# Kernel optimization log

Hardware: AMD Instinct MI355X
Metric: run time of the kernel (lower is better)

Reference implementation:

```python
import jax, jax.numpy as jnp
import numpy as np
import math

B, S, D, H, HD, R, F = 2, 2048, 1024, 16, 64, 32, 4096
EPS = 1e-5

def _layernorm(x, g, b):
    mu = jnp.mean(x, axis=-1, keepdims=True)
    var = jnp.mean(jnp.square(x - mu), axis=-1, keepdims=True)
    return (x - mu) * jax.lax.rsqrt(var + EPS) * g + b

def _gelu(x):
    # faithful tanh-approximation from the module
    c = math.sqrt(2.0 / math.pi)
    return 0.5 * x * (1.0 + jnp.tanh(c * (x + 0.044715 * x ** 3)))

def setup_inputs() -> dict:
    key = jax.random.key(0)
    ks = jax.random.split(key, 8)
    s = 0.02
    return dict(
        x=jax.random.normal(ks[0], (B, S, D), jnp.float32),
        ln1_g=jnp.ones((D,), jnp.float32), ln1_b=jnp.zeros((D,), jnp.float32),
        Wq=jax.random.normal(ks[1], (H, D, HD), jnp.float32) * s,
        bq=jnp.zeros((H, HD), jnp.float32),
        Wk=jax.random.normal(ks[2], (H, D, HD), jnp.float32) * s,
        bk=jnp.zeros((H, HD), jnp.float32),
        Wvd=jax.random.normal(ks[3], (H, D, R), jnp.float32) * s,
        bvd=jnp.zeros((H, R), jnp.float32),
        Wvu=jax.random.normal(ks[4], (H, R, HD), jnp.float32) * s,
        bvu=jnp.zeros((H, HD), jnp.float32),
        ln2_g=jnp.ones((D,), jnp.float32), ln2_b=jnp.zeros((D,), jnp.float32),
        W1=jax.random.normal(ks[5], (D, F), jnp.float32) * s,
        b1=jnp.zeros((F,), jnp.float32),
        W2=jax.random.normal(ks[6], (F, D), jnp.float32) * s,
        b2=jnp.zeros((D,), jnp.float32),
    )

def reference(x, ln1_g, ln1_b, Wq, bq, Wk, bk, Wvd, bvd, Wvu, bvu,
              ln2_g, ln2_b, W1, b1, W2, b2):
    Bx, Sx, Dx = x.shape
    y = x
    h = _layernorm(x, ln1_g, ln1_b)
    # all heads batched: [B,H,S,HD]
    q = jnp.einsum('bsd,hde->bhse', h, Wq) + bq[None, :, None, :]
    k = jnp.einsum('bsd,hde->bhse', h, Wk) + bk[None, :, None, :]
    vd = jnp.einsum('bsd,hdr->bhsr', h, Wvd) + bvd[None, :, None, :]
    v = jnp.einsum('bhsr,hre->bhse', vd, Wvu) + bvu[None, :, None, :]
    scores = jnp.einsum('bhse,bhte->bhst', q, k) / math.sqrt(Dx)  # NB: scaled by embed dim, as in source
    i = jnp.arange(Sx)
    mask = i[None, :] < i[:, None]  # key index < query index is masked (reversed causal, faithful)
    scores = jnp.where(mask[None, None, :, :], -jnp.inf, scores)
    attn = jax.nn.softmax(scores, axis=-1)
    o = jnp.einsum('bhst,bhte->bhse', attn, v)
    o = o.transpose(0, 2, 1, 3).reshape(Bx, Sx, Dx)  # concat heads
    x = o + y
    y = x
    h = _layernorm(x, ln2_g, ln2_b)
    h = _gelu(h @ W1 + b1)
    h = h @ W2 + b2
    return h + y
```

## Files before the change

kernel.cpp:

```cpp
#include <hip/hip_runtime.h>


typedef unsigned short u16;
typedef __attribute__((ext_vector_type(4))) float f32x4;
typedef __attribute__((ext_vector_type(8))) __bf16 bf16x8;

#define B_ 2
#define S_ 2048
#define D_ 1024
#define H_ 16
#define HD_ 64
#define R_ 32
#define F_ 4096
#define M_ (B_ * S_)
#define NQKV 2560
#define C2F 0.04508422002778011f

__device__ __forceinline__ u16 f2bf(float f) {
  union { float f; unsigned u; } v; v.f = f;
  unsigned u = v.u;
  return (u16)((u + 0x7FFFu + ((u >> 16) & 1u)) >> 16);
}
__device__ __forceinline__ float bf2f(u16 h) {
  union { unsigned u; float f; } v; v.u = ((unsigned)h) << 16;
  return v.f;
}
__device__ __forceinline__ unsigned pk_bf16(float lo, float hi) {
  unsigned r;
  asm volatile("v_cvt_pk_bf16_f32 %0, %1, %2" : "=v"(r) : "v"(lo), "v"(hi));
  return r;
}

typedef __attribute__((address_space(1))) void gvoid;
typedef __attribute__((address_space(3))) void lvoid;
__device__ __forceinline__ void gload_lds16(const void* g, void* l) {
  __builtin_amdgcn_global_load_lds((gvoid*)(void*)g, (lvoid*)l, 16, 0, 0);
}

__device__ __forceinline__ float gelu_f(float x) {
  float t = tanhf(0.7978845608028654f * (x + 0.044715f * x * x * x));
  return 0.5f * x * (1.0f + t);
}

__global__ __launch_bounds__(256) void wtrans(const float* __restrict__ in,
                                              u16* __restrict__ out,
                                              int Rr, int Cc, long ibs, long obs,
                                              float scale) {
  __shared__ float tile[32][33];
  const float* ip = in + (size_t)blockIdx.z * ibs;
  u16* op = out + (size_t)blockIdx.z * obs;
  int c0 = blockIdx.x * 32, r0 = blockIdx.y * 32;
  int tx = threadIdx.x & 31, ty = threadIdx.x >> 5;
#pragma unroll
  for (int j = 0; j < 32; j += 8)
    tile[ty + j][tx] = ip[(size_t)(r0 + ty + j) * Cc + c0 + tx];
  __syncthreads();
#pragma unroll
  for (int j = 0; j < 32; j += 8)
    op[(size_t)(c0 + ty + j) * Rr + r0 + tx] = f2bf(tile[tx][ty + j] * scale);
}

__global__ __launch_bounds__(256) void wconv(const float* __restrict__ in,
                                             u16* __restrict__ out, int n) {
  int i = (blockIdx.x * 256 + threadIdx.x) * 4;
  if (i < n) {
    float4 v = *(const float4*)&in[i];
    ushort4 o;
    o.x = f2bf(v.x); o.y = f2bf(v.y); o.z = f2bf(v.z); o.w = f2bf(v.w);
    *(ushort4*)&out[i] = o;
  }
}

__global__ __launch_bounds__(256) void bconcat(const float* __restrict__ bq,
                                               const float* __restrict__ bk,
                                               const float* __restrict__ bvd,
                                               float* __restrict__ o) {
  int i = blockIdx.x * 256 + threadIdx.x;
  if (i < NQKV) {
    float v = (i < 1024) ? bq[i] * C2F : (i < 2048 ? bk[i - 1024] : bvd[i - 2048]);
    o[i] = v;
  }
}

__global__ __launch_bounds__(256) void ln_kernel(const float* __restrict__ xin,
                                                 const float* __restrict__ addin,
                                                 const float* __restrict__ gam,
                                                 const float* __restrict__ bet,
                                                 u16* __restrict__ hout,
                                                 float* __restrict__ x2out) {
  int row = blockIdx.x, tid = threadIdx.x;
  size_t base = (size_t)row * D_ + tid * 4;
  float4 v = *(const float4*)&xin[base];
  if (addin) {
    float4 a = *(const float4*)&addin[base];
    v.x += a.x; v.y += a.y; v.z += a.z; v.w += a.w;
  }
  if (x2out) *(float4*)&x2out[base] = v;
  float s = v.x + v.y + v.z + v.w;
  float ss = v.x * v.x + v.y * v.y + v.z * v.z + v.w * v.w;
#pragma unroll
  for (int off = 32; off > 0; off >>= 1) {
    s += __shfl_down(s, off);
    ss += __shfl_down(ss, off);
  }
  __shared__ float red[8];
  int wv = tid >> 6;
  if ((tid & 63) == 0) { red[wv] = s; red[4 + wv] = ss; }
  __syncthreads();
  if (tid == 0) {
    float s1 = red[0] + red[1] + red[2] + red[3];
    float s2 = red[4] + red[5] + red[6] + red[7];
    float mu = s1 * (1.0f / D_);
    red[0] = mu;
    red[1] = s2 * (1.0f / D_) - mu * mu;
  }
  __syncthreads();
  float mu = red[0];
  float rstd = rsqrtf(red[1] + 1e-5f);
  int ci = tid * 4;
  ushort4 o;
  o.x = f2bf((v.x - mu) * rstd * gam[ci + 0] + bet[ci + 0]);
  o.y = f2bf((v.y - mu) * rstd * gam[ci + 1] + bet[ci + 1]);
  o.z = f2bf((v.z - mu) * rstd * gam[ci + 2] + bet[ci + 2]);
  o.w = f2bf((v.w - mu) * rstd * gam[ci + 3] + bet[ci + 3]);
  *(ushort4*)&hout[base] = o;
}

template <int MODE>
__global__ __launch_bounds__(256) void gemm_nt(const u16* __restrict__ A,
                                               const u16* __restrict__ Bt,
                                               int K, int lda, int ldb,
                                               const float* __restrict__ bias,
                                               const float* __restrict__ res,
                                               void* __restrict__ Cout,
                                               void* __restrict__ Cout2, int ldc) {
  __shared__ __align__(16) u16 As0[128 * 32];
  __shared__ __align__(16) u16 Bs0[128 * 32];
  __shared__ __align__(16) u16 As1[128 * 32];
  __shared__ __align__(16) u16 Bs1[128 * 32];
  int tid = threadIdx.x;
  int lane = tid & 63, wid = tid >> 6;
  int wm = wid >> 1, wn = wid & 1;
  int row0 = blockIdx.y * 128, col0 = blockIdx.x * 128;
  int l15 = lane & 15, g = lane >> 4;
  int srow = lane >> 2, scol = (lane & 3) * 8;
  f32x4 acc[4][4] = {};
  const u16* Ap = A + (size_t)row0 * lda;
  const u16* Bp = Bt + (size_t)col0 * ldb;

  auto STAGE = [&](u16* AS, u16* BS, int kk) {
#pragma unroll
    for (int i = 0; i < 2; ++i) {
      int c = wid * 2 + i;
      gload_lds16(Ap + (size_t)(c * 16 + srow) * lda + kk + scol, &AS[c * 512]);
      gload_lds16(Bp + (size_t)(c * 16 + srow) * ldb + kk + scol, &BS[c * 512]);
    }
  };
  auto COMPUTE = [&](const u16* AS, const u16* BS) {
    bf16x8 af[4], bfr[4];
#pragma unroll
    for (int t = 0; t < 4; ++t) {
      af[t] = *(const bf16x8*)&AS[(wm * 64 + t * 16 + l15) * 32 + g * 8];
      bfr[t] = *(const bf16x8*)&BS[(wn * 64 + t * 16 + l15) * 32 + g * 8];
    }
#pragma unroll
    for (int mt = 0; mt < 4; ++mt)
#pragma unroll
      for (int nt = 0; nt < 4; ++nt)
        acc[mt][nt] = __builtin_amdgcn_mfma_f32_16x16x32_bf16(af[mt], bfr[nt],
                                                              acc[mt][nt], 0, 0, 0);
  };

  STAGE(As0, Bs0, 0);
  __syncthreads();
  for (int k0 = 0; k0 < K; k0 += 64) {
    if (k0 + 32 < K) STAGE(As1, Bs1, k0 + 32);
    COMPUTE(As0, Bs0);
    __syncthreads();
    if (k0 + 64 < K) STAGE(As0, Bs0, k0 + 64);
    COMPUTE(As1, Bs1);
    __syncthreads();
  }

#pragma unroll
  for (int mt = 0; mt < 4; ++mt) {
#pragma unroll
    for (int nt = 0; nt < 4; ++nt) {
      int cc = col0 + wn * 64 + nt * 16 + l15;
      float bv = bias ? bias[cc] : 0.0f;
#pragma unroll
      for (int j = 0; j < 4; ++j) {
        int rr = row0 + wm * 64 + mt * 16 + g * 4 + j;
        float v = acc[mt][nt][j] + bv;
        if (MODE == 1) v = gelu_f(v);
        if (MODE == 2) {
          ((float*)Cout)[(size_t)rr * ldc + cc] = v + res[(size_t)rr * ldc + cc];
        } else {
          ((u16*)Cout)[(size_t)rr * ldc + cc] = f2bf(v);
        }
      }
    }
  }
  (void)Cout2;
}

template <int MODE>
__global__ __launch_bounds__(512, 2) void gemm8(
    const u16* __restrict__ A, const u16* __restrict__ Bt,
    int lda, int ldb, int nk,
    const float* __restrict__ bias,
    float* __restrict__ Cf, u16* __restrict__ Cb,
    u16* __restrict__ P1, u16* __restrict__ P2, u16* __restrict__ P3,
    int ldc) {
  extern __shared__ __align__(16) char smem[];
  int tid = threadIdx.x;
  int lane = tid & 63, wid = tid >> 6;
  int wm = wid >> 2, wn = wid & 3;
  int l15 = lane & 15, g = lane >> 4;
  int row0 = blockIdx.y * 256, col0 = blockIdx.x * 256;
  int koff = (MODE == 4) ? blockIdx.z * (nk * 64) : 0;
  const u16* Ap = A + (size_t)row0 * lda + koff;
  const u16* Bp = Bt + (size_t)col0 * ldb + koff;
  int trow = tid >> 3;
  int sbyte = ((tid & 7) * 16) ^ ((trow & 7) << 4);
  int xr = (l15 & 7) << 4;

  f32x4 acc[8][4] = {};

  auto STAGE = [&](int slot, int kt) {
#pragma unroll
    for (int l = 0; l < 4; ++l)
      gload_lds16((const char*)(Ap + (size_t)(l * 64 + trow) * lda + kt) + sbyte,
                  smem + slot * 65536 + (l * 64 + wid * 8) * 128);
#pragma unroll
    for (int l = 0; l < 4; ++l)
      gload_lds16((const char*)(Bp + (size_t)(l * 64 + trow) * ldb + kt) + sbyte,
                  smem + slot * 65536 + 32768 + (l * 64 + wid * 8) * 128);
  };

  STAGE(0, 0);
  STAGE(1, 64);

  for (int it = 0; it < nk; ++it) {
    if (it + 1 < nk) {
      asm volatile("s_waitcnt vmcnt(8)" ::: "memory");
    } else {
      asm volatile("s_waitcnt vmcnt(0)" ::: "memory");
    }
    __builtin_amdgcn_sched_barrier(0);
    __builtin_amdgcn_s_barrier();
    __builtin_amdgcn_sched_barrier(0);

    const char* Ab = smem + (it & 1) * 65536 + (size_t)(wm * 128 + l15) * 128;
    const char* Bb = smem + (it & 1) * 65536 + 32768 + (size_t)(wn * 64 + l15) * 128;
#pragma unroll
    for (int kk = 0; kk < 2; ++kk) {
      int kq = (kk * 64 + g * 16) ^ xr;
      bf16x8 bfr[4], af[8];
#pragma unroll
      for (int nt = 0; nt < 4; ++nt)
        bfr[nt] = *(const bf16x8*)(Bb + nt * 2048 + kq);
#pragma unroll
      for (int mt = 0; mt < 8; ++mt)
        af[mt] = *(const bf16x8*)(Ab + mt * 2048 + kq);
      __builtin_amdgcn_s_setprio(1);
#pragma unroll
      for (int mt = 0; mt < 8; ++mt)
#pragma unroll
        for (int nt = 0; nt < 4; ++nt)
          acc[mt][nt] = __builtin_amdgcn_mfma_f32_16x16x32_bf16(af[mt], bfr[nt],
                                                                acc[mt][nt], 0, 0, 0);
      __builtin_amdgcn_s_setprio(0);
    }

    __builtin_amdgcn_s_barrier();
    __builtin_amdgcn_sched_barrier(0);
    if (it + 2 < nk) STAGE(it & 1, (it + 2) * 64);
  }

  u16* pp = (u16*)nullptr;
  if (MODE == 4 && blockIdx.z != 0)
    pp = (blockIdx.z == 1) ? P1 : (blockIdx.z == 2 ? P2 : P3);
#pragma unroll
  for (int mt = 0; mt < 8; ++mt) {
#pragma unroll
    for (int nt = 0; nt < 4; ++nt) {
      int cc = col0 + wn * 64 + nt * 16 + l15;
      float bv = (MODE == 1) ? bias[cc] : 0.0f;
#pragma unroll
      for (int j = 0; j < 4; ++j) {
        int rr = row0 + wm * 128 + mt * 16 + g * 4 + j;
        float v = acc[mt][nt][j] + bv;
        if (MODE == 1) {
          Cb[(size_t)rr * ldc + cc] = f2bf(gelu_f(v));
        } else {
          if (blockIdx.z == 0) Cf[(size_t)rr * ldc + cc] = v;
          else                 pp[(size_t)rr * ldc + cc] = f2bf(v);
        }
      }
    }
  }
}

__global__ __launch_bounds__(256) void reduce2(float* __restrict__ out,
                                               const u16* __restrict__ p1,
                                               const u16* __restrict__ p2,
                                               const u16* __restrict__ p3,
                                               const float* __restrict__ b2,
                                               const float* __restrict__ x2) {
  int i = (blockIdx.x * 256 + threadIdx.x) * 4;
  float4 o = *(float4*)&out[i];
  ushort4 a = *(const ushort4*)&p1[i];
  ushort4 b = *(const ushort4*)&p2[i];
  ushort4 c = *(const ushort4*)&p3[i];
  float4 r = *(const float4*)&x2[i];
  int cix = i & (D_ - 1);
  o.x += bf2f(a.x) + bf2f(b.x) + bf2f(c.x) + b2[cix + 0] + r.x;
  o.y += bf2f(a.y) + bf2f(b.y) + bf2f(c.y) + b2[cix + 1] + r.y;
  o.z += bf2f(a.z) + bf2f(b.z) + bf2f(c.z) + b2[cix + 2] + r.z;
  o.w += bf2f(a.w) + bf2f(b.w) + bf2f(c.w) + b2[cix + 3] + r.w;
  *(float4*)&out[i] = o;
}

__global__ __launch_bounds__(256) void vu_kernel(const u16* __restrict__ vd,
                                                 const u16* __restrict__ wvu,
                                                 const float* __restrict__ bvu,
                                                 u16* __restrict__ v_t) {
  int t0 = blockIdx.x * 64, h = blockIdx.y, b = blockIdx.z;
  __shared__ u16 vds[64][32];
  __shared__ u16 vt[64][65];
  int tid = threadIdx.x;
  {
    int rr2 = tid >> 2, c8 = (tid & 3) * 8;
    *(bf16x8*)&vds[rr2][c8] =
        *(const bf16x8*)&vd[(size_t)(b * S_ + t0 + rr2) * NQKV + 2048 + h * R_ + c8];
  }
  __syncthreads();
  int e = tid & 63, tg = (tid >> 6) * 16;
  float wcol[32];
#pragma unroll
  for (int r = 0; r < 32; ++r) wcol[r] = bf2f(wvu[((size_t)h * R_ + r) * HD_ + e]);
  float bb = bvu[h * HD_ + e];
  for (int i = 0; i < 16; ++i) {
    int t = tg + i;
    float acc = bb;
#pragma unroll
    for (int r = 0; r < 32; ++r) acc += bf2f(vds[t][r]) * wcol[r];
    vt[t][e] = f2bf(acc);
  }
  __syncthreads();
  for (int idx = tid; idx < 64 * 64; idx += 256) {
    int e2 = idx >> 6, t2 = idx & 63;
    v_t[((size_t)(b * H_ + h) * HD_ + e2) * S_ + t0 + t2] = vt[t2][e2];
  }
}

__global__ __launch_bounds__(512, 2) void attn_kernel(const u16* __restrict__ cqkv,
                                                      const u16* __restrict__ v_t,
                                                      float* __restrict__ o) {
  extern __shared__ __align__(16) u16 kv[];
  __shared__ u16 Pl[8][16 * 64];
  int tid = threadIdx.x;
  int lane = tid & 63, w = tid >> 6;
  int h = blockIdx.x, b = blockIdx.y;
  int bx = blockIdx.z;
  int r = lane & 15, g = lane >> 4;
  const u16* qp = cqkv + (size_t)(b * S_) * NQKV + h * HD_;
  const u16* kp = cqkv + (size_t)(b * S_) * NQKV + 1024 + h * HD_;
  const u16* vp = v_t + (size_t)(b * H_ + h) * HD_ * S_;
  u16* Pw = Pl[w];

  int srow = w * 8 + (lane >> 3);
  int ssw = ((lane & 7) * 16) ^ (((lane >> 3) & 7) << 4);

  int xr = (r & 7) << 4;
  int kq0 = ((g * 16) ^ xr) >> 1;
  int kq1 = ((64 + g * 16) ^ xr) >> 1;

  auto STAGE = [&](int buf, int kt) {
    u16* base = kv + buf * 8192;
    gload_lds16((const char*)(kp + (size_t)(kt + srow) * NQKV) + ssw,
                base + w * 512);
    gload_lds16((const char*)(vp + (size_t)srow * S_ + kt) + ssw,
                base + 4096 + w * 512);
  };

#pragma unroll 1
  for (int half = 0; half < 2; ++half) {
    int qb = half ? (S_ - 128) - bx * 128 : bx * 128;
    int s0 = qb + w * 16;
    int qrow = s0 + r;

    gload_lds16((const char*)(qp + (size_t)(s0 + (lane >> 3)) * NQKV) + ssw, Pw);
    gload_lds16((const char*)(qp + (size_t)(s0 + 8 + (lane >> 3)) * NQKV) + ssw,
                Pw + 512);
    asm volatile("s_waitcnt vmcnt(0)" ::: "memory");
    __builtin_amdgcn_sched_barrier(0);
    __builtin_amdgcn_s_barrier();
    __builtin_amdgcn_sched_barrier(0);
    bf16x8 aq0 = *(const bf16x8*)&Pw[(r << 6) + kq0];
    bf16x8 aq1 = *(const bf16x8*)&Pw[(r << 6) + kq1];

    f32x4 oa[4] = {};
    float m_ = -1e30f, l_ = 0.0f;

    int nt = (S_ - qb) >> 6;
    STAGE(0, qb);
    STAGE(1, qb + 64);

    for (int it = 0; it < nt; ++it) {
      int kt = qb + it * 64;
      if (it + 1 < nt) {
        asm volatile("s_waitcnt vmcnt(2)" ::: "memory");
      } else {
        asm volatile("s_waitcnt vmcnt(0)" ::: "memory");
      }
      __builtin_amdgcn_sched_barrier(0);
      __builtin_amdgcn_s_barrier();
      __builtin_amdgcn_sched_barrier(0);
      if (it + 2 < nt) STAGE((it + 2) % 3, qb + (it + 2) * 64);

      if (kt + 64 > s0) {
        const u16* Kb = kv + (it % 3) * 8192;
        const u16* Vb = Kb + 4096;

        f32x4 sc[4] = {};
#pragma unroll
        for (int blk = 0; blk < 4; ++blk) {
          bf16x8 a0 = *(const bf16x8*)&Kb[((blk * 16 + r) << 6) + kq0];
          bf16x8 a1 = *(const bf16x8*)&Kb[((blk * 16 + r) << 6) + kq1];
          sc[blk] = __builtin_amdgcn_mfma_f32_16x16x32_bf16(a0, aq0, sc[blk], 0, 0, 0);
          sc[blk] = __builtin_amdgcn_mfma_f32_16x16x32_bf16(a1, aq1, sc[blk], 0, 0, 0);
        }

        float p[16];
        if ((qrow & ~63) == kt) {
#pragma unroll
          for (int blk = 0; blk < 4; ++blk)
#pragma unroll
            for (int j = 0; j < 4; ++j) {
              int kk = kt + blk * 16 + g * 4 + j;
              p[blk * 4 + j] = (kk < qrow) ? -1e30f : sc[blk][j];
            }
        } else {
#pragma unroll
          for (int blk = 0; blk < 4; ++blk)
#pragma unroll
            for (int j = 0; j < 4; ++j) p[blk * 4 + j] = sc[blk][j];
        }
        float mx = p[0];
#pragma unroll
        for (int i = 1; i < 16; ++i) mx = fmaxf(mx, p[i]);
        mx = fmaxf(mx, __shfl_xor(mx, 16));
        mx = fmaxf(mx, __shfl_xor(mx, 32));
        float mn = fmaxf(m_, mx);
        float scl = __builtin_amdgcn_exp2f(m_ - mn);
        m_ = mn;
        float sm = 0.0f;
#pragma unroll
        for (int i = 0; i < 16; ++i) {
          p[i] = __builtin_amdgcn_exp2f(p[i] - mn);
          sm += p[i];
        }
        sm += __shfl_xor(sm, 16);
        sm += __shfl_xor(sm, 32);
        l_ = l_ * scl + sm;
#pragma unroll
        for (int et = 0; et < 4; ++et) oa[et] *= scl;

#pragma unroll
        for (int blk = 0; blk < 4; ++blk) {
          uint2 pk;
          pk.x = pk_bf16(p[blk * 4 + 0], p[blk * 4 + 1]);
          pk.y = pk_bf16(p[blk * 4 + 2], p[blk * 4 + 3]);
          *(uint2*)&Pw[(r << 6) + ((((blk << 5) + (g << 3)) ^ xr) >> 1)] = pk;
        }
        asm volatile("s_waitcnt lgkmcnt(0)" ::: "memory");
        __builtin_amdgcn_sched_barrier(0);
        bf16x8 pb0 = *(const bf16x8*)&Pw[(r << 6) + kq0];
        bf16x8 pb1 = *(const bf16x8*)&Pw[(r << 6) + kq1];
#pragma unroll
        for (int et = 0; et < 4; ++et) {
          bf16x8 v0 = *(const bf16x8*)&Vb[((et * 16 + r) << 6) + kq0];
          bf16x8 v1 = *(const bf16x8*)&Vb[((et * 16 + r) << 6) + kq1];
          oa[et] = __builtin_amdgcn_mfma_f32_16x16x32_bf16(v0, pb0, oa[et], 0, 0, 0);
          oa[et] = __builtin_amdgcn_mfma_f32_16x16x32_bf16(v1, pb1, oa[et], 0, 0, 0);
        }
      }
    }

    float inv = 1.0f / l_;
#pragma unroll
    for (int et = 0; et < 4; ++et)
#pragma unroll
      for (int j = 0; j < 4; ++j)
        o[(size_t)(b * S_ + s0 + r) * D_ + h * HD_ + et * 16 + g * 4 + j] =
            oa[et][j] * inv;
  }
}

namespace {
struct GemmAttrInit {
  GemmAttrInit() {
    hipFuncSetAttribute((const void*)gemm8<1>,
                        hipFuncAttributeMaxDynamicSharedMemorySize, 131072);
    hipFuncSetAttribute((const void*)gemm8<4>,
                        hipFuncAttributeMaxDynamicSharedMemorySize, 131072);
    hipFuncSetAttribute((const void*)attn_kernel,
                        hipFuncAttributeMaxDynamicSharedMemorySize, 49152);
  }
};
GemmAttrInit _gemm_attr_init;
}

extern "C" void kernel_launch(void* const* d_in, const int* in_sizes, int n_in,
                              void* d_out, int out_size, void* d_ws, size_t ws_size,
                              hipStream_t stream) {
  const float* x = (const float*)d_in[0];
  const float* ln1_g = (const float*)d_in[1];
  const float* ln1_b = (const float*)d_in[2];
  const float* Wq = (const float*)d_in[3];
  const float* bq = (const float*)d_in[4];
  const float* Wk = (const float*)d_in[5];
  const float* bk = (const float*)d_in[6];
  const float* Wvd = (const float*)d_in[7];
  const float* bvd = (const float*)d_in[8];
  const float* Wvu = (const float*)d_in[9];
  const float* bvu = (const float*)d_in[10];
  const float* ln2_g = (const float*)d_in[11];
  const float* ln2_b = (const float*)d_in[12];
  const float* W1 = (const float*)d_in[13];
  const float* b1 = (const float*)d_in[14];
  const float* W2 = (const float*)d_in[15];
  const float* b2 = (const float*)d_in[16];
  float* out = (float*)d_out;
  (void)in_sizes; (void)n_in; (void)out_size; (void)ws_size;

  char* ws = (char*)d_ws;
  const size_t MB = 1024 * 1024;
  const size_t KB = 1024;
  u16* wqkvT = (u16*)(ws + 0);
  u16* wvuB = (u16*)(ws + 5 * MB);
  float* bqkv = (float*)(ws + 5 * MB + 64 * KB);
  u16* w1T = (u16*)(ws + 5 * MB + 384 * KB);
  u16* w2T = (u16*)(ws + 13 * MB + 384 * KB);
  u16* hbuf = (u16*)(ws + 21 * MB + 384 * KB);
  u16* cqkv = (u16*)(ws + 29 * MB + 384 * KB);
  u16* vT = (u16*)(ws + 49 * MB + 384 * KB);
  float* ob = (float*)(ws + 57 * MB + 384 * KB);
  float* x2 = (float*)(ws + 73 * MB + 384 * KB);
  u16* ubuf = cqkv;
  u16* p1 = (u16*)(ws + 0);
  u16* p2 = (u16*)hbuf;
  u16* p3 = (u16*)vT;

  dim3 blk(256);
  wtrans<<<dim3(2, 32, 16), blk, 0, stream>>>(Wq, wqkvT, 1024, 64, 65536L, 65536L, C2F);
  wtrans<<<dim3(2, 32, 16), blk, 0, stream>>>(Wk, wqkvT + 1024 * 1024, 1024, 64,
                                              65536L, 65536L, 1.0f);
  wtrans<<<dim3(1, 32, 16), blk, 0, stream>>>(Wvd, wqkvT + 2048 * 1024, 1024, 32,
                                              32768L, 32768L, 1.0f);
  wconv<<<dim3(32), blk, 0, stream>>>(Wvu, wvuB, H_ * R_ * HD_);
  bconcat<<<dim3(10), blk, 0, stream>>>(bq, bk, bvd, bqkv);
  wtrans<<<dim3(128, 32, 1), blk, 0, stream>>>(W1, w1T, 1024, 4096, 0L, 0L, 1.0f);
  wtrans<<<dim3(32, 128, 1), blk, 0, stream>>>(W2, w2T, 4096, 1024, 0L, 0L, 1.0f);
  ln_kernel<<<dim3(M_), blk, 0, stream>>>(x, (const float*)nullptr, ln1_g, ln1_b,
                                          hbuf, (float*)nullptr);
  gemm_nt<0><<<dim3(20, 32), blk, 0, stream>>>(hbuf, wqkvT, 1024, 1024, 1024, bqkv,
                                               (const float*)nullptr, (void*)cqkv,
                                               (void*)nullptr, NQKV);
  vu_kernel<<<dim3(S_ / 64, H_, B_), blk, 0, stream>>>(cqkv, wvuB, bvu, vT);
  attn_kernel<<<dim3(H_, B_, 8), dim3(512), 49152, stream>>>(cqkv, vT, ob);
  ln_kernel<<<dim3(M_), blk, 0, stream>>>(x, ob, ln2_g, ln2_b, hbuf, x2);
  gemm8<1><<<dim3(16, 16, 1), dim3(512), 131072, stream>>>(
      hbuf, w1T, 1024, 1024, 16, b1, (float*)nullptr, ubuf,
      (u16*)nullptr, (u16*)nullptr, (u16*)nullptr, 4096);
  gemm8<4><<<dim3(4, 16, 4), dim3(512), 131072, stream>>>(
      ubuf, w2T, 4096, 4096, 16, (const float*)nullptr, out, (u16*)nullptr,
      p1, p2, p3, 1024);
  reduce2<<<dim3(M_ * D_ / 1024), blk, 0, stream>>>(out, p1, p2, p3, b2, x2);
}
```

Before: 233.2 us.

## Interleave GEMM tile prefetch with MFMA quarters using finer-grained staging

```diff
diff --git a/kernel.cpp b/kernel.cpp
--- a/kernel.cpp
+++ b/kernel.cpp
@@ -224,58 +224,102 @@
   int trow = tid >> 3;
   int sbyte = ((tid & 7) * 16) ^ ((trow & 7) << 4);
   int xr = (l15 & 7) << 4;
+  int kq0 = (g * 16) ^ xr;
+  int kq1 = (64 + g * 16) ^ xr;
 
   f32x4 acc[8][4] = {};
 
-  auto STAGE = [&](int slot, int kt) {
-#pragma unroll
-    for (int l = 0; l < 4; ++l)
-      gload_lds16((const char*)(Ap + (size_t)(l * 64 + trow) * lda + kt) + sbyte,
-                  smem + slot * 65536 + (l * 64 + wid * 8) * 128);
-#pragma unroll
-    for (int l = 0; l < 4; ++l)
-      gload_lds16((const char*)(Bp + (size_t)(l * 64 + trow) * ldb + kt) + sbyte,
-                  smem + slot * 65536 + 32768 + (l * 64 + wid * 8) * 128);
+  auto STAGE_A = [&](int t, int h) {
+#pragma unroll
+    for (int l = 2 * h; l < 2 * h + 2; ++l)
+      gload_lds16((const char*)(Ap + (size_t)(l * 64 + trow) * lda + t * 64) + sbyte,
+                  smem + (t & 1) * 65536 + (l * 64 + wid * 8) * 128);
   };
-
-  STAGE(0, 0);
-  STAGE(1, 64);
-
-  for (int it = 0; it < nk; ++it) {
-    if (it + 1 < nk) {
-      asm volatile("s_waitcnt vmcnt(8)" ::: "memory");
+  auto STAGE_B = [&](int t, int h) {
+#pragma unroll
+    for (int l = 2 * h; l < 2 * h + 2; ++l)
+      gload_lds16((const char*)(Bp + (size_t)(l * 64 + trow) * ldb + t * 64) + sbyte,
+                  smem + (t & 1) * 65536 + 32768 + (l * 64 + wid * 8) * 128);
+  };
+
+  STAGE_A(0, 0); STAGE_A(0, 1); STAGE_B(0, 0); STAGE_B(0, 1);
+
+  for (int t = 0; t < nk; ++t) {
+    const char* Ab = smem + (t & 1) * 65536 + (size_t)(wm * 128 + l15) * 128;
+    const char* Bb = smem + (t & 1) * 65536 + 32768 + (size_t)(wn * 64 + l15) * 128;
+    bool pf = (t + 1 < nk);
+    bf16x8 af[8], bfr[4];
+
+    if (pf) {
+      STAGE_A(t + 1, 0);
+      asm volatile("s_waitcnt vmcnt(2)" ::: "memory");
     } else {
       asm volatile("s_waitcnt vmcnt(0)" ::: "memory");
     }
     __builtin_amdgcn_sched_barrier(0);
     __builtin_amdgcn_s_barrier();
     __builtin_amdgcn_sched_barrier(0);
-
-    const char* Ab = smem + (it & 1) * 65536 + (size_t)(wm * 128 + l15) * 128;
-    const char* Bb = smem + (it & 1) * 65536 + 32768 + (size_t)(wn * 64 + l15) * 128;
-#pragma unroll
-    for (int kk = 0; kk < 2; ++kk) {
-      int kq = (kk * 64 + g * 16) ^ xr;
-      bf16x8 bfr[4], af[8];
-#pragma unroll
-      for (int nt = 0; nt < 4; ++nt)
-        bfr[nt] = *(const bf16x8*)(Bb + nt * 2048 + kq);
-#pragma unroll
-      for (int mt = 0; mt < 8; ++mt)
-        af[mt] = *(const bf16x8*)(Ab + mt * 2048 + kq);
-      __builtin_amdgcn_s_setprio(1);
-#pragma unroll
-      for (int mt = 0; mt < 8; ++mt)
-#pragma unroll
-        for (int nt = 0; nt < 4; ++nt)
-          acc[mt][nt] = __builtin_amdgcn_mfma_f32_16x16x32_bf16(af[mt], bfr[nt],
-                                                                acc[mt][nt], 0, 0, 0);
-      __builtin_amdgcn_s_setprio(0);
-    }
-
-    __builtin_amdgcn_s_barrier();
-    __builtin_amdgcn_sched_barrier(0);
-    if (it + 2 < nk) STAGE(it & 1, (it + 2) * 64);
+#pragma unroll
+    for (int mt = 0; mt < 8; ++mt) af[mt] = *(const bf16x8*)(Ab + mt * 2048 + kq0);
+    bfr[0] = *(const bf16x8*)(Bb + 0 * 2048 + kq0);
+    bfr[1] = *(const bf16x8*)(Bb + 1 * 2048 + kq0);
+    asm volatile("s_waitcnt lgkmcnt(0)" ::: "memory");
+    __builtin_amdgcn_sched_barrier(0);
+    __builtin_amdgcn_s_setprio(1);
+#pragma unroll
+    for (int mt = 0; mt < 8; ++mt) {
+      acc[mt][0] = __builtin_amdgcn_mfma_f32_16x16x32_bf16(af[mt], bfr[0], acc[mt][0], 0, 0, 0);
+      acc[mt][1] = __builtin_amdgcn_mfma_f32_16x16x32_bf16(af[mt], bfr[1], acc[mt][1], 0, 0, 0);
+    }
+    __builtin_amdgcn_s_setprio(0);
+    __builtin_amdgcn_s_barrier();
+
+    bfr[2] = *(const bf16x8*)(Bb + 2 * 2048 + kq0);
+    bfr[3] = *(const bf16x8*)(Bb + 3 * 2048 + kq0);
+    if (pf) STAGE_A(t + 1, 1);
+    __builtin_amdgcn_s_barrier();
+    asm volatile("s_waitcnt lgkmcnt(0)" ::: "memory");
+    __builtin_amdgcn_sched_barrier(0);
+    __builtin_amdgcn_s_setprio(1);
+#pragma unroll
+    for (int mt = 0; mt < 8; ++mt) {
+      acc[mt][2] = __builtin_amdgcn_mfma_f32_16x16x32_bf16(af[mt], bfr[2], acc[mt][2], 0, 0, 0);
+      acc[mt][3] = __builtin_amdgcn_mfma_f32_16x16x32_bf16(af[mt], bfr[3], acc[mt][3], 0, 0, 0);
+    }
+    __builtin_amdgcn_s_setprio(0);
+    __builtin_amdgcn_s_barrier();
+
+#pragma unroll
+    for (int mt = 0; mt < 8; ++mt) af[mt] = *(const bf16x8*)(Ab + mt * 2048 + kq1);
+    bfr[0] = *(const bf16x8*)(Bb + 0 * 2048 + kq1);
+    bfr[1] = *(const bf16x8*)(Bb + 1 * 2048 + kq1);
+    if (pf) STAGE_B(t + 1, 0);
+    __builtin_amdgcn_s_barrier();
+    asm volatile("s_waitcnt lgkmcnt(0)" ::: "memory");
+    __builtin_amdgcn_sched_barrier(0);
+    __builtin_amdgcn_s_setprio(1);
+#pragma unroll
+    for (int mt = 0; mt < 8; ++mt) {
+      acc[mt][0] = __builtin_amdgcn_mfma_f32_16x16x32_bf16(af[mt], bfr[0], acc[mt][0], 0, 0, 0);
+      acc[mt][1] = __builtin_amdgcn_mfma_f32_16x16x32_bf16(af[mt], bfr[1], acc[mt][1], 0, 0, 0);
+    }
+    __builtin_amdgcn_s_setprio(0);
+    __builtin_amdgcn_s_barrier();
+
+    bfr[2] = *(const bf16x8*)(Bb + 2 * 2048 + kq1);
+    bfr[3] = *(const bf16x8*)(Bb + 3 * 2048 + kq1);
+    if (pf) STAGE_B(t + 1, 1);
+    __builtin_amdgcn_s_barrier();
+    asm volatile("s_waitcnt lgkmcnt(0)" ::: "memory");
+    __builtin_amdgcn_sched_barrier(0);
+    __builtin_amdgcn_s_setprio(1);
+#pragma unroll
+    for (int mt = 0; mt < 8; ++mt) {
+      acc[mt][2] = __builtin_amdgcn_mfma_f32_16x16x32_bf16(af[mt], bfr[2], acc[mt][2], 0, 0, 0);
+      acc[mt][3] = __builtin_amdgcn_mfma_f32_16x16x32_bf16(af[mt], bfr[3], acc[mt][3], 0, 0, 0);
+    }
+    __builtin_amdgcn_s_setprio(0);
+    __builtin_amdgcn_s_barrier();
   }
 
   u16* pp = (u16*)nullptr;
```

After: 230.6 us. No clear change (-1.1%).
